# Performance work log

Hardware: AMD Instinct MI355X
Metric: run time of the kernel (lower is better)

Reference implementation:

```python
import jax, jax.numpy as jnp
import numpy as np

TEMPERATURE = 0.5


def setup_inputs() -> dict:
    key = jax.random.key(0)
    k1, k2 = jax.random.split(key)
    B, D = 4096, 256
    z_i = jax.random.normal(k1, (B, D), dtype=jnp.float32)
    z_j = jax.random.normal(k2, (B, D), dtype=jnp.float32)
    return {"z_i": z_i, "z_j": z_j}


def reference(z_i, z_j):
    B = z_i.shape[0]
    N = 2 * B
    z = jnp.concatenate([z_i, z_j], axis=0)                      # [N, D]
    # cosine similarity = normalized dot products (fused: normalize + matmul)
    zn = z / jnp.linalg.norm(z, axis=-1, keepdims=True)
    sim = jnp.einsum('nd,md->nm', zn, zn) / TEMPERATURE          # [N, N]
    # positives: sim[i, i+B] and sim[i+B, i]
    idx = jnp.arange(B)
    pos = jnp.concatenate([sim[idx, idx + B], sim[idx + B, idx]])  # [N]
    # cross-entropy with label 0 over logits [pos, negatives]:
    # logsumexp over row excluding only the diagonal (positive counted once)
    neg_inf = jnp.asarray(-jnp.inf, sim.dtype)
    sim_masked = jnp.where(jnp.eye(N, dtype=bool), neg_inf, sim)
    lse = jax.nn.logsumexp(sim_masked, axis=1)                    # [N]
    loss = jnp.sum(lse - pos) / N
    return loss
```

## Files before the change

### kernel.cpp

```cpp
#include <hip/hip_runtime.h>

typedef __attribute__((ext_vector_type(4))) float f32x4;
typedef __attribute__((ext_vector_type(2))) long long i64x2;

static constexpr int D = 256;
static constexpr float INV_T = 2.0f;
static constexpr float KEXP2 = 2.8853900817779268f;
static constexpr int TTILE = 64;
static constexpr int NBLK = TTILE * (TTILE + 1) / 2;
static constexpr int NPLANE = 2 * TTILE;
static constexpr int LSE_BLOCKS = 32;

__device__ inline float fexp2(float x) {
#if __has_builtin(__builtin_amdgcn_exp2f)
    return __builtin_amdgcn_exp2f(x);
#else
    return exp2f(x);
#endif
}
__device__ inline unsigned int cvt4_fp8(float a, float b, float c, float d) {
    int v = __builtin_amdgcn_cvt_pk_fp8_f32(a, b, 0, false);
    v = __builtin_amdgcn_cvt_pk_fp8_f32(c, d, v, true);
    return (unsigned int)v;
}

__global__ void k_norm(const float* __restrict__ zi, const float* __restrict__ zj,
                       unsigned char* __restrict__ zn, float* __restrict__ diag,
                       float* __restrict__ pos_partial, unsigned int* __restrict__ counter,
                       int B) {
    __shared__ float red[4];
    const int lane = threadIdx.x & 63;
    const int wv = threadIdx.x >> 6;
    const int i = blockIdx.x * 4 + wv;
    if (blockIdx.x == 0 && threadIdx.x == 0) *counter = 0;
    if (i < B) {
        float4 vi = reinterpret_cast<const float4*>(zi + (size_t)i * D)[lane];
        float4 vj = reinterpret_cast<const float4*>(zj + (size_t)i * D)[lane];
        float ssi = vi.x * vi.x + vi.y * vi.y + vi.z * vi.z + vi.w * vi.w;
        float ssj = vj.x * vj.x + vj.y * vj.y + vj.z * vj.z + vj.w * vj.w;
#pragma unroll
        for (int off = 32; off >= 1; off >>= 1) {
            ssi += __shfl_xor(ssi, off, 64);
            ssj += __shfl_xor(ssj, off, 64);
        }
        float rni = rsqrtf(ssi), rnj = rsqrtf(ssj);
        unsigned int pa = cvt4_fp8(vi.x * rni, vi.y * rni, vi.z * rni, vi.w * rni);
        unsigned int pb = cvt4_fp8(vj.x * rnj, vj.y * rnj, vj.z * rnj, vj.w * rnj);
        float fa0 = __builtin_amdgcn_cvt_f32_fp8((int)pa, 0);
        float fa1 = __builtin_amdgcn_cvt_f32_fp8((int)pa, 1);
        float fa2 = __builtin_amdgcn_cvt_f32_fp8((int)pa, 2);
        float fa3 = __builtin_amdgcn_cvt_f32_fp8((int)pa, 3);
        float fb0 = __builtin_amdgcn_cvt_f32_fp8((int)pb, 0);
        float fb1 = __builtin_amdgcn_cvt_f32_fp8((int)pb, 1);
        float fb2 = __builtin_amdgcn_cvt_f32_fp8((int)pb, 2);
        float fb3 = __builtin_amdgcn_cvt_f32_fp8((int)pb, 3);
        float sdi = fa0 * fa0 + fa1 * fa1 + fa2 * fa2 + fa3 * fa3;
        float sdj = fb0 * fb0 + fb1 * fb1 + fb2 * fb2 + fb3 * fb3;
        float pd  = fa0 * fb0 + fa1 * fb1 + fa2 * fb2 + fa3 * fb3;
#pragma unroll
        for (int off = 32; off >= 1; off >>= 1) {
            sdi += __shfl_xor(sdi, off, 64);
            sdj += __shfl_xor(sdj, off, 64);
            pd  += __shfl_xor(pd, off, 64);
        }
        unsigned int qa = __shfl_xor(pa, 1, 64);
        unsigned int qb = __shfl_xor(pb, 1, 64);
        if ((lane & 1) == 0) {
            int m = lane >> 1;
            size_t base = (size_t)(m >> 3) * 1024 + (size_t)((m & 3) * 16) * 16
                        + (size_t)(((m >> 2) & 1)) * 8;
            size_t offA = (size_t)(i >> 4) * 4096 + base + (size_t)(i & 15) * 16;
            int ib = i + B;
            size_t offB = (size_t)(ib >> 4) * 4096 + base + (size_t)(ib & 15) * 16;
            *reinterpret_cast<unsigned long long*>(zn + offA) =
                ((unsigned long long)qa << 32) | pa;
            *reinterpret_cast<unsigned long long*>(zn + offB) =
                ((unsigned long long)qb << 32) | pb;
        }
        if (lane == 0) {
            diag[i]     = -fexp2(KEXP2 * sdi);
            diag[i + B] = -fexp2(KEXP2 * sdj);
            red[wv] = pd;
        }
    } else if (lane == 0) {
        red[wv] = 0.f;
    }
    __syncthreads();
    if (threadIdx.x == 0)
        pos_partial[blockIdx.x] = 2.0f * INV_T * (red[0] + red[1] + red[2] + red[3]);
}

__global__ __launch_bounds__(256, 2)
void k_main(const unsigned char* __restrict__ zn, float* __restrict__ P, int N) {
    const int tid = threadIdx.x;
    const int lane = tid & 63, wv = tid >> 6;
    const int l15 = lane & 15, lhi = lane >> 4;
    const int wr = wv >> 1, wc = wv & 1;

    const int bid = (int)blockIdx.x;
    const int swz = (bid & 7) * (NBLK / 8) + (bid >> 3);
    int ti = (int)(((float)(2 * TTILE + 1) -
                    sqrtf((float)((2 * TTILE + 1) * (2 * TTILE + 1)) - 8.0f * (float)swz)) * 0.5f);
    ti = (ti < 0) ? 0 : ((ti > TTILE - 1) ? TTILE - 1 : ti);
#pragma unroll 2
    while (ti > 0 && (ti * TTILE - ((ti * (ti - 1)) >> 1)) > swz) --ti;
#pragma unroll 2
    while (((ti + 1) * TTILE - (((ti + 1) * ti) >> 1)) <= swz) ++ti;
    const int tj = ti + (swz - (ti * TTILE - ((ti * (ti - 1)) >> 1)));

    const i64x2* Ap = reinterpret_cast<const i64x2*>(zn + (size_t)ti * 32768);
    const i64x2* Bp = reinterpret_cast<const i64x2*>(zn + (size_t)tj * 32768);

    i64x2 a_[4][4], b_[4][4];
#pragma unroll
    for (int kkp = 0; kkp < 4; ++kkp)
#pragma unroll
        for (int r = 0; r < 4; ++r) {
            a_[kkp][r] = Ap[((wr * 4 + r) * 4 + kkp) * 64 + lane];
            b_[kkp][r] = Bp[((wc * 4 + r) * 4 + kkp) * 64 + lane];
        }

    f32x4 acc[4][4];
#pragma unroll
    for (int r = 0; r < 4; ++r)
#pragma unroll
        for (int c = 0; c < 4; ++c) acc[r][c] = (f32x4){0.f, 0.f, 0.f, 0.f};

#pragma unroll
    for (int kkp = 0; kkp < 4; ++kkp) {
#pragma unroll
        for (int r = 0; r < 4; ++r)
#pragma unroll
            for (int c = 0; c < 4; ++c)
                acc[r][c] = __builtin_amdgcn_mfma_f32_16x16x32_fp8_fp8(
                    a_[kkp][r].x, b_[kkp][c].x, acc[r][c], 0, 0, 0);
#pragma unroll
        for (int r = 0; r < 4; ++r)
#pragma unroll
            for (int c = 0; c < 4; ++c)
                acc[r][c] = __builtin_amdgcn_mfma_f32_16x16x32_fp8_fp8(
                    a_[kkp][r].y, b_[kkp][c].y, acc[r][c], 0, 0, 0);
    }

    float cs[4] = {0.f, 0.f, 0.f, 0.f};
#pragma unroll
    for (int r = 0; r < 4; ++r) {
        float rq0 = 0.f, rq1 = 0.f, rq2 = 0.f, rq3 = 0.f;
#pragma unroll
        for (int c = 0; c < 4; ++c) {
            float e0 = fexp2(KEXP2 * acc[r][c][0]);
            float e1 = fexp2(KEXP2 * acc[r][c][1]);
            float e2 = fexp2(KEXP2 * acc[r][c][2]);
            float e3 = fexp2(KEXP2 * acc[r][c][3]);
            rq0 += e0; rq1 += e1; rq2 += e2; rq3 += e3;
            cs[c] += e0 + e1 + e2 + e3;
        }
#pragma unroll
        for (int off = 1; off <= 8; off <<= 1) {
            rq0 += __shfl_xor(rq0, off, 64);
            rq1 += __shfl_xor(rq1, off, 64);
            rq2 += __shfl_xor(rq2, off, 64);
            rq3 += __shfl_xor(rq3, off, 64);
        }
        if (l15 == 0) {
            f32x4 out = (f32x4){rq0, rq1, rq2, rq3};
            *reinterpret_cast<f32x4*>(
                P + (size_t)(2 * tj + wc) * N + ti * 128 + wr * 64 + r * 16 + lhi * 4) = out;
        }
    }
    if (ti != tj) {
#pragma unroll
        for (int c = 0; c < 4; ++c) {
            float v = cs[c];
            v += __shfl_xor(v, 16, 64);
            v += __shfl_xor(v, 32, 64);
            if (lhi == 0)
                P[(size_t)(2 * ti + wr) * N + tj * 128 + wc * 64 + c * 16 + l15] = v;
        }
    }
}

__global__ void k_lse(const float* __restrict__ P, const float* __restrict__ diag,
                      const float* __restrict__ pos_partial, int n_pos,
                      float* __restrict__ part, unsigned int* __restrict__ counter,
                      float* __restrict__ out, int N) {
    __shared__ float red[4];
    const int lane = threadIdx.x & 63, wv = threadIdx.x >> 6;
    const int row = blockIdx.x * 256 + threadIdx.x;
    float s = diag[row];
#pragma unroll 8
    for (int k = 0; k < NPLANE; ++k) s += P[(size_t)k * N + row];
    float local = __logf(s);
#pragma unroll
    for (int off = 32; off >= 1; off >>= 1) local += __shfl_xor(local, off, 64);
    if (lane == 0) red[wv] = local;
    __syncthreads();
    bool last = false;
    if (threadIdx.x == 0) {
        part[blockIdx.x] = red[0] + red[1] + red[2] + red[3];
        __threadfence();
        last = (atomicAdd(counter, 1u) == LSE_BLOCKS - 1);
    }
    __shared__ int lastflag;
    if (threadIdx.x == 0) lastflag = last ? 1 : 0;
    __syncthreads();
    if (lastflag) {
        __threadfence();
        float t = 0.f;
        for (int i = threadIdx.x; i < LSE_BLOCKS; i += 256) t += part[i];
        for (int i = threadIdx.x; i < n_pos; i += 256) t -= pos_partial[i];
#pragma unroll
        for (int off = 32; off >= 1; off >>= 1) t += __shfl_xor(t, off, 64);
        if (lane == 0) red[wv] = t;
        __syncthreads();
        if (threadIdx.x == 0)
            out[0] = (red[0] + red[1] + red[2] + red[3]) / (float)N;
    }
}

extern "C" void kernel_launch(void* const* d_in, const int* in_sizes, int n_in,
                              void* d_out, int out_size, void* d_ws, size_t ws_size,
                              hipStream_t stream) {
    const float* zi = (const float*)d_in[0];
    const float* zj = (const float*)d_in[1];
    const int B = in_sizes[0] / D;
    const int N = 2 * B;

    char* ws = (char*)d_ws;
    unsigned char* zn = (unsigned char*)ws;
    float* diag = (float*)(ws + (size_t)N * D);
    float* pos_partial = diag + N;
    float* part = pos_partial + 1024;
    unsigned int* counter = (unsigned int*)(part + 32);
    float* P = part + 64;

    float* out = (float*)d_out;

    const int npb = B / 4;
    hipLaunchKernelGGL(k_norm, dim3(npb), dim3(256), 0, stream, zi, zj, zn, diag,
                       pos_partial, counter, B);
    hipLaunchKernelGGL(k_main, dim3(NBLK), dim3(256), 0, stream, zn, P, N);
    hipLaunchKernelGGL(k_lse, dim3(LSE_BLOCKS), dim3(256), 0, stream, P, diag,
                       pos_partial, npb, part, counter, out, N);
}
```

Baseline: 41.44 us.

## Reshape similarity tiles to two-wave blocks and parallelize LSE row reduction

```diff
diff --git a/kernel.cpp b/kernel.cpp
--- a/kernel.cpp
+++ b/kernel.cpp
@@ -7,9 +7,9 @@
 static constexpr float INV_T = 2.0f;
 static constexpr float KEXP2 = 2.8853900817779268f;
 static constexpr int TTILE = 64;
-static constexpr int NBLK = TTILE * (TTILE + 1) / 2;
+static constexpr int NT = TTILE * (TTILE + 1) / 2;
 static constexpr int NPLANE = 2 * TTILE;
-static constexpr int LSE_BLOCKS = 32;
+static constexpr int LSE_BLOCKS = 256;
 
 __device__ inline float fexp2(float x) {
 #if __has_builtin(__builtin_amdgcn_exp2f)
@@ -90,61 +90,59 @@
         pos_partial[blockIdx.x] = 2.0f * INV_T * (red[0] + red[1] + red[2] + red[3]);
 }
 
-__global__ __launch_bounds__(256, 2)
+__global__ __launch_bounds__(128, 2)
 void k_main(const unsigned char* __restrict__ zn, float* __restrict__ P, int N) {
     const int tid = threadIdx.x;
-    const int lane = tid & 63, wv = tid >> 6;
+    const int lane = tid & 63;
+    const int wc = tid >> 6;
     const int l15 = lane & 15, lhi = lane >> 4;
-    const int wr = wv >> 1, wc = wv & 1;
 
     const int bid = (int)blockIdx.x;
-    const int swz = (bid & 7) * (NBLK / 8) + (bid >> 3);
+    const int swz = (bid & 7) * (NT / 8) + (bid >> 3);
     int ti = (int)(((float)(2 * TTILE + 1) -
                     sqrtf((float)((2 * TTILE + 1) * (2 * TTILE + 1)) - 8.0f * (float)swz)) * 0.5f);
     ti = (ti < 0) ? 0 : ((ti > TTILE - 1) ? TTILE - 1 : ti);
-#pragma unroll 2
     while (ti > 0 && (ti * TTILE - ((ti * (ti - 1)) >> 1)) > swz) --ti;
-#pragma unroll 2
     while (((ti + 1) * TTILE - (((ti + 1) * ti) >> 1)) <= swz) ++ti;
     const int tj = ti + (swz - (ti * TTILE - ((ti * (ti - 1)) >> 1)));
 
     const i64x2* Ap = reinterpret_cast<const i64x2*>(zn + (size_t)ti * 32768);
     const i64x2* Bp = reinterpret_cast<const i64x2*>(zn + (size_t)tj * 32768);
 
-    i64x2 a_[4][4], b_[4][4];
-#pragma unroll
-    for (int kkp = 0; kkp < 4; ++kkp)
-#pragma unroll
-        for (int r = 0; r < 4; ++r) {
-            a_[kkp][r] = Ap[((wr * 4 + r) * 4 + kkp) * 64 + lane];
-            b_[kkp][r] = Bp[((wc * 4 + r) * 4 + kkp) * 64 + lane];
-        }
-
-    f32x4 acc[4][4];
-#pragma unroll
-    for (int r = 0; r < 4; ++r)
+    f32x4 acc[8][4];
+#pragma unroll
+    for (int r = 0; r < 8; ++r)
 #pragma unroll
         for (int c = 0; c < 4; ++c) acc[r][c] = (f32x4){0.f, 0.f, 0.f, 0.f};
 
 #pragma unroll
     for (int kkp = 0; kkp < 4; ++kkp) {
-#pragma unroll
-        for (int r = 0; r < 4; ++r)
+        i64x2 a_[8], b_[4];
+#pragma unroll
+        for (int r = 0; r < 8; ++r)
+            a_[r] = Ap[(r * 4 + kkp) * 64 + lane];
+#pragma unroll
+        for (int c = 0; c < 4; ++c)
+            b_[c] = Bp[((wc * 4 + c) * 4 + kkp) * 64 + lane];
+        __builtin_amdgcn_s_setprio(1);
+#pragma unroll
+        for (int r = 0; r < 8; ++r)
 #pragma unroll
             for (int c = 0; c < 4; ++c)
                 acc[r][c] = __builtin_amdgcn_mfma_f32_16x16x32_fp8_fp8(
-                    a_[kkp][r].x, b_[kkp][c].x, acc[r][c], 0, 0, 0);
-#pragma unroll
-        for (int r = 0; r < 4; ++r)
+                    a_[r].x, b_[c].x, acc[r][c], 0, 0, 0);
+#pragma unroll
+        for (int r = 0; r < 8; ++r)
 #pragma unroll
             for (int c = 0; c < 4; ++c)
                 acc[r][c] = __builtin_amdgcn_mfma_f32_16x16x32_fp8_fp8(
-                    a_[kkp][r].y, b_[kkp][c].y, acc[r][c], 0, 0, 0);
+                    a_[r].y, b_[c].y, acc[r][c], 0, 0, 0);
+        __builtin_amdgcn_s_setprio(0);
     }
 
     float cs[4] = {0.f, 0.f, 0.f, 0.f};
 #pragma unroll
-    for (int r = 0; r < 4; ++r) {
+    for (int r = 0; r < 8; ++r) {
         float rq0 = 0.f, rq1 = 0.f, rq2 = 0.f, rq3 = 0.f;
 #pragma unroll
         for (int c = 0; c < 4; ++c) {
@@ -163,9 +161,9 @@
             rq3 += __shfl_xor(rq3, off, 64);
         }
         if (l15 == 0) {
-            f32x4 out = (f32x4){rq0, rq1, rq2, rq3};
+            f32x4 o = (f32x4){rq0, rq1, rq2, rq3};
             *reinterpret_cast<f32x4*>(
-                P + (size_t)(2 * tj + wc) * N + ti * 128 + wr * 64 + r * 16 + lhi * 4) = out;
+                P + (size_t)(2 * tj + wc) * N + ti * 128 + r * 16 + lhi * 4) = o;
         }
     }
     if (ti != tj) {
@@ -175,7 +173,7 @@
             v += __shfl_xor(v, 16, 64);
             v += __shfl_xor(v, 32, 64);
             if (lhi == 0)
-                P[(size_t)(2 * ti + wr) * N + tj * 128 + wc * 64 + c * 16 + l15] = v;
+                P[(size_t)(2 * ti + wc) * N + tj * 128 + wc * 64 + c * 16 + l15] = v;
         }
     }
 }
@@ -185,35 +183,42 @@
                       float* __restrict__ part, unsigned int* __restrict__ counter,
                       float* __restrict__ out, int N) {
     __shared__ float red[4];
-    const int lane = threadIdx.x & 63, wv = threadIdx.x >> 6;
-    const int row = blockIdx.x * 256 + threadIdx.x;
-    float s = diag[row];
-#pragma unroll 8
-    for (int k = 0; k < NPLANE; ++k) s += P[(size_t)k * N + row];
-    float local = __logf(s);
-#pragma unroll
-    for (int off = 32; off >= 1; off >>= 1) local += __shfl_xor(local, off, 64);
-    if (lane == 0) red[wv] = local;
+    const int tid = threadIdx.x;
+    const int lane = tid & 63, wv = tid >> 6;
+    const int row = blockIdx.x * 32 + (tid >> 3);
+    const int sub = tid & 7;
+    float s = 0.f;
+#pragma unroll
+    for (int d = 0; d < 16; ++d)
+        s += P[(size_t)(sub * 16 + d) * N + row];
+    s += __shfl_xor(s, 1, 64);
+    s += __shfl_xor(s, 2, 64);
+    s += __shfl_xor(s, 4, 64);
+    float lg = (sub == 0) ? __logf(s + diag[row]) : 0.f;
+    lg += __shfl_xor(lg, 8, 64);
+    lg += __shfl_xor(lg, 16, 64);
+    lg += __shfl_xor(lg, 32, 64);
+    if (lane == 0) red[wv] = lg;
     __syncthreads();
     bool last = false;
-    if (threadIdx.x == 0) {
+    if (tid == 0) {
         part[blockIdx.x] = red[0] + red[1] + red[2] + red[3];
         __threadfence();
         last = (atomicAdd(counter, 1u) == LSE_BLOCKS - 1);
     }
     __shared__ int lastflag;
-    if (threadIdx.x == 0) lastflag = last ? 1 : 0;
+    if (tid == 0) lastflag = last ? 1 : 0;
     __syncthreads();
     if (lastflag) {
         __threadfence();
         float t = 0.f;
-        for (int i = threadIdx.x; i < LSE_BLOCKS; i += 256) t += part[i];
-        for (int i = threadIdx.x; i < n_pos; i += 256) t -= pos_partial[i];
+        for (int i = tid; i < LSE_BLOCKS; i += 256) t += part[i];
+        for (int i = tid; i < n_pos; i += 256) t -= pos_partial[i];
 #pragma unroll
         for (int off = 32; off >= 1; off >>= 1) t += __shfl_xor(t, off, 64);
         if (lane == 0) red[wv] = t;
         __syncthreads();
-        if (threadIdx.x == 0)
+        if (tid == 0)
             out[0] = (red[0] + red[1] + red[2] + red[3]) / (float)N;
     }
 }
@@ -231,15 +236,16 @@
     float* diag = (float*)(ws + (size_t)N * D);
     float* pos_partial = diag + N;
     float* part = pos_partial + 1024;
-    unsigned int* counter = (unsigned int*)(part + 32);
-    float* P = part + 64;
+    unsigned int* counter = (unsigned int*)(part + 256);
+    float* P = (float*)(counter + 32);
 
     float* out = (float*)d_out;
 
     const int npb = B / 4;
+    hipMemsetAsync(P, 0, (size_t)NPLANE * N * sizeof(float), stream);
     hipLaunchKernelGGL(k_norm, dim3(npb), dim3(256), 0, stream, zi, zj, zn, diag,
                        pos_partial, counter, B);
-    hipLaunchKernelGGL(k_main, dim3(NBLK), dim3(256), 0, stream, zn, P, N);
+    hipLaunchKernelGGL(k_main, dim3(NT), dim3(128), 0, stream, zn, P, N);
     hipLaunchKernelGGL(k_lse, dim3(LSE_BLOCKS), dim3(256), 0, stream, P, diag,
                        pos_partial, npb, part, counter, out, N);
 }
```

Measured after the change: 48.74 us. +17.6%, slower.
